# Optimization experiments

Measured on AMD Instinct MI355X. Metric: run time of the kernel, lower is better.

Reference implementation:

```python
import jax, jax.numpy as jnp
import numpy as np

HIDDEN = 1024
NUM_HEAD = 16
HEAD_DIM = HIDDEN // NUM_HEAD


def setup_inputs() -> dict:
    key = jax.random.key(0)
    ks = jax.random.split(key, 12)
    bs, seq = 4, 2048
    inp = {
        'srcQ': jax.random.normal(ks[0], (bs, seq, HIDDEN), jnp.float32),
        'srcK': jax.random.normal(ks[1], (bs, seq, HIDDEN), jnp.float32),
        'srcV': jax.random.normal(ks[2], (bs, seq, HIDDEN), jnp.float32),
        'mask': jnp.ones((bs, 1, 1, seq), jnp.int32),
        'Wq': jax.random.normal(ks[3], (HIDDEN, HIDDEN), jnp.float32) * 0.02,
        'bq': jnp.zeros((HIDDEN,), jnp.float32),
        'Wk': jax.random.normal(ks[4], (HIDDEN, HIDDEN), jnp.float32) * 0.02,
        'bk': jnp.zeros((HIDDEN,), jnp.float32),
        'Wv': jax.random.normal(ks[5], (HIDDEN, HIDDEN), jnp.float32) * 0.02,
        'bv': jnp.zeros((HIDDEN,), jnp.float32),
        'Wo': jax.random.normal(ks[6], (HIDDEN, HIDDEN), jnp.float32) * 0.02,
        'bo': jnp.zeros((HIDDEN,), jnp.float32),
    }
    return inp


def _split_heads(x):
    # [bs, seq, hidden] -> [bs, num_head, seq, head_dim]
    bs, seq, _ = x.shape
    return x.reshape(bs, seq, NUM_HEAD, HEAD_DIM).transpose(0, 2, 1, 3)


def reference(srcQ, srcK, srcV, mask, Wq, bq, Wk, bk, Wv, bv, Wo, bo):
    Q = _split_heads(srcQ @ Wq + bq)
    K = _split_heads(srcK @ Wk + bk)
    V = _split_heads(srcV @ Wv + bv)
    # NOTE: original module applies NO 1/sqrt(d) scaling (scale tensor unused)
    scores = jnp.einsum('bhqd,bhkd->bhqk', Q, K)
    scores = jnp.where(mask == 0, jnp.float32(-10000.0), scores)
    attn = jax.nn.softmax(scores, axis=-1)  # dropout is identity in eval
    out = jnp.einsum('bhqk,bhkd->bhqd', attn, V)
    bs, _, seq, _ = out.shape
    out = out.transpose(0, 2, 1, 3).reshape(bs, seq, HIDDEN)
    return out @ Wo + bo
```

## Files before the change

### kernel.cpp

```cpp
#include <hip/hip_runtime.h>

typedef short bf16x8 __attribute__((ext_vector_type(8)));
typedef short bf16x4 __attribute__((ext_vector_type(4)));
typedef float f32x4 __attribute__((ext_vector_type(4)));
typedef unsigned short ushort8 __attribute__((ext_vector_type(8)));
typedef unsigned short ushort4v __attribute__((ext_vector_type(4)));
typedef unsigned int uint4v __attribute__((ext_vector_type(4)));
typedef float float4v __attribute__((ext_vector_type(4)));

#define LOG2E 1.4426950408889634f
#define MASKED_VAL -14426.950408889634f

__device__ __forceinline__ unsigned short f2bf(float f) {
  unsigned u = __builtin_bit_cast(unsigned, f);
  u = u + 0x7fffu + ((u >> 16) & 1u);
  return (unsigned short)(u >> 16);
}

__device__ __forceinline__ unsigned pk2(float a, float b) {
  unsigned r;
  asm("v_cvt_pk_bf16_f32 %0, %1, %2" : "=v"(r) : "v"(a), "v"(b));
  return r;
}

__device__ __forceinline__ float exp2a(float x) {
  float r;
  asm("v_exp_f32 %0, %1" : "=v"(r) : "v"(x));
  return r;
}

__device__ __forceinline__ void gload16(const void* g, void* l) {
  __builtin_amdgcn_global_load_lds(
      (const __attribute__((address_space(1))) unsigned int*)g,
      (__attribute__((address_space(3))) unsigned int*)l, 16, 0, 0);
}

__global__ __launch_bounds__(256) void transpose_w4(const float* __restrict__ W0,
                                                    const float* __restrict__ W1,
                                                    const float* __restrict__ W2,
                                                    const float* __restrict__ W3,
                                                    unsigned short* __restrict__ Wt) {
  __shared__ float tile[32][33];
  const int z = blockIdx.z;
  const float* W = (z == 0) ? W0 : (z == 1) ? W1 : (z == 2) ? W2 : W3;
  unsigned short* o = Wt + (size_t)z * (1 << 20);
  int bx = blockIdx.x * 32;
  int by = blockIdx.y * 32;
  int tx = threadIdx.x & 31;
  int ty = threadIdx.x >> 5;
#pragma unroll
  for (int j = 0; j < 32; j += 8)
    tile[ty + j][tx] = W[(size_t)(by + ty + j) * 1024 + bx + tx];
  __syncthreads();
#pragma unroll
  for (int j = 0; j < 32; j += 8)
    o[(size_t)(bx + ty + j) * 1024 + by + tx] = f2bf(tile[tx][ty + j]);
}

__global__ __launch_bounds__(256, 3) void gemm_qkv(
    const float* __restrict__ srcQ, const float* __restrict__ srcK,
    const float* __restrict__ srcV, const unsigned short* __restrict__ Wt,
    const float* __restrict__ bq, const float* __restrict__ bk,
    const float* __restrict__ bv, unsigned short* __restrict__ Qb,
    unsigned short* __restrict__ Kb, unsigned short* __restrict__ Vt) {
  __shared__ __align__(16) unsigned short As[3][128 * 32];
  __shared__ __align__(16) unsigned short Bs[3][128 * 32];
  const int K = 1024, N = 1024;
  const int chunk = blockIdx.x >> 9;
  const int inner = blockIdx.x & 511;
  const int x = inner & 7, i = inner >> 3;
  const int bm = (x << 3) + (i >> 3);
  const int bn = i & 7;
  const float* Af = (chunk == 0) ? srcQ : (chunk == 1) ? srcK : srcV;
  const unsigned short* Bt = Wt + (size_t)chunk * (1 << 20);
  const float* bias = (chunk == 0) ? bq : (chunk == 1) ? bk : bv;
  const float scale = (chunk == 0) ? LOG2E : 1.0f;
  const int t = threadIdx.x;
  const int lane = t & 63, wid = t >> 6;
  const int wr = wid >> 1, wc = wid & 1;
  const int lr = lane & 15, lg = lane >> 4;
  f32x4 acc[4][4] = {};
  const size_t baseA = (size_t)(bm * 128) * K;
  const size_t baseB = (size_t)(bn * 128) * K;
  const int c0 = t, c1 = t + 256;
  const size_t a0off = baseA + (size_t)(c0 >> 2) * K + (c0 & 3) * 8;
  const size_t a1off = baseA + (size_t)(c1 >> 2) * K + (c1 & 3) * 8;
  const size_t b0off = baseB + (size_t)(c0 >> 2) * K + (c0 & 3) * 8;
  const size_t b1off = baseB + (size_t)(c1 >> 2) * K + (c1 & 3) * 8;

  unsigned short* pA0 = &As[0][0];
  unsigned short* pA1 = &As[1][0];
  unsigned short* pA2 = &As[2][0];
  unsigned short* pB0 = &Bs[0][0];
  unsigned short* pB1 = &Bs[1][0];
  unsigned short* pB2 = &Bs[2][0];
  float4v fE[4], fO[4];

  auto loadA = [&](float4v* f, int ks) {
    f[0] = *(const float4v*)&Af[a0off + ks];
    f[1] = *(const float4v*)&Af[a0off + ks + 4];
    f[2] = *(const float4v*)&Af[a1off + ks];
    f[3] = *(const float4v*)&Af[a1off + ks + 4];
  };
  auto writeA = [&](const float4v* f, unsigned short* dst) {
    uint4v w0, w1;
    w0[0] = pk2(f[0][0], f[0][1]); w0[1] = pk2(f[0][2], f[0][3]);
    w0[2] = pk2(f[1][0], f[1][1]); w0[3] = pk2(f[1][2], f[1][3]);
    w1[0] = pk2(f[2][0], f[2][1]); w1[1] = pk2(f[2][2], f[2][3]);
    w1[2] = pk2(f[3][0], f[3][1]); w1[3] = pk2(f[3][2], f[3][3]);
    *(uint4v*)&dst[c0 * 8] = w0;
    *(uint4v*)&dst[c1 * 8] = w1;
  };
  auto compute = [&]() {
    bf16x8 a[4], b[4];
#pragma unroll
    for (int m = 0; m < 4; ++m)
      a[m] = *(const bf16x8*)&pA0[(wr * 64 + 16 * m + lr) * 32 + lg * 8];
#pragma unroll
    for (int n = 0; n < 4; ++n)
      b[n] = *(const bf16x8*)&pB0[(wc * 64 + 16 * n + lr) * 32 + lg * 8];
    __builtin_amdgcn_s_setprio(1);
#pragma unroll
    for (int m = 0; m < 4; ++m)
#pragma unroll
      for (int n = 0; n < 4; ++n)
        acc[m][n] = __builtin_amdgcn_mfma_f32_16x16x32_bf16(a[m], b[n], acc[m][n], 0, 0, 0);
    __builtin_amdgcn_s_setprio(0);
  };
  auto rotate = [&]() {
    unsigned short* ta = pA0; pA0 = pA1; pA1 = pA2; pA2 = ta;
    unsigned short* tb = pB0; pB0 = pB1; pB1 = pB2; pB2 = tb;
  };

  gload16(&Bt[b0off], &pB0[c0 * 8]);
  gload16(&Bt[b1off], &pB0[c1 * 8]);
  loadA(fE, 0);
  gload16(&Bt[b0off + 32], &pB1[c0 * 8]);
  gload16(&Bt[b1off + 32], &pB1[c1 * 8]);
  loadA(fO, 32);
  writeA(fE, pA0);
  asm volatile("s_waitcnt lgkmcnt(0)" ::: "memory");
  __builtin_amdgcn_s_barrier();

  for (int it = 0; it < 16; ++it) {
    const int ks0 = 64 * it;
    if (it < 15) {
      gload16(&Bt[b0off + ks0 + 64], &pB2[c0 * 8]);
      gload16(&Bt[b1off + ks0 + 64], &pB2[c1 * 8]);
      loadA(fE, ks0 + 64);
    }
    compute();
    writeA(fO, pA1);
    asm volatile("s_waitcnt lgkmcnt(0)" ::: "memory");
    __builtin_amdgcn_sched_barrier(0);
    __builtin_amdgcn_s_barrier();
    rotate();
    if (it < 15) {
      gload16(&Bt[b0off + ks0 + 96], &pB2[c0 * 8]);
      gload16(&Bt[b1off + ks0 + 96], &pB2[c1 * 8]);
      loadA(fO, ks0 + 96);
    }
    compute();
    if (it < 15) {
      writeA(fE, pA1);
      asm volatile("s_waitcnt lgkmcnt(0)" ::: "memory");
      __builtin_amdgcn_sched_barrier(0);
      __builtin_amdgcn_s_barrier();
      rotate();
    }
  }

  const int rowb = bm * 128 + wr * 64;
  const int colb = bn * 128 + wc * 64;
  if (chunk == 2) {
    const int bidx = rowb >> 11;
    const int srow = rowb & 2047;
#pragma unroll
    for (int n = 0; n < 4; ++n) {
      int col = colb + 16 * n + lr;
      float bv_ = bias[col];
#pragma unroll
      for (int m = 0; m < 4; ++m) {
        int s0 = srow + 16 * m + 4 * lg;
        ushort4v u;
#pragma unroll
        for (int r = 0; r < 4; ++r) u[r] = f2bf(acc[m][n][r] + bv_);
        *(ushort4v*)&Vt[((size_t)(bidx * 1024 + col)) * 2048 + s0] = u;
      }
    }
  } else {
    unsigned short* C = (chunk == 0) ? Qb : Kb;
#pragma unroll
    for (int n = 0; n < 4; ++n) {
      int col = colb + 16 * n + lr;
      float bv_ = bias[col];
#pragma unroll
      for (int m = 0; m < 4; ++m) {
        int row0 = rowb + 16 * m + 4 * lg;
#pragma unroll
        for (int r = 0; r < 4; ++r)
          C[(size_t)(row0 + r) * N + col] = f2bf((acc[m][n][r] + bv_) * scale);
      }
    }
  }
}

__global__ __launch_bounds__(256, 3) void gemm_out(const unsigned short* __restrict__ A,
                                                   const unsigned short* __restrict__ Bt,
                                                   const float* __restrict__ bias,
                                                   float* __restrict__ C) {
  __shared__ __align__(16) unsigned short As[3][128 * 32];
  __shared__ __align__(16) unsigned short Bs[3][128 * 32];
  const int K = 1024, N = 1024;
  const int x = blockIdx.x & 7, i = blockIdx.x >> 3;
  const int bm = (x << 3) + (i >> 3);
  const int bn = i & 7;
  const int t = threadIdx.x;
  const int lane = t & 63, wid = t >> 6;
  const int wr = wid >> 1, wc = wid & 1;
  const int lr = lane & 15, lg = lane >> 4;
  f32x4 acc[4][4] = {};
  const size_t baseA = (size_t)(bm * 128) * K;
  const size_t baseB = (size_t)(bn * 128) * K;
  const int c0 = t, c1 = t + 256;
  const size_t a0off = baseA + (size_t)(c0 >> 2) * K + (c0 & 3) * 8;
  const size_t a1off = baseA + (size_t)(c1 >> 2) * K + (c1 & 3) * 8;
  const size_t b0off = baseB + (size_t)(c0 >> 2) * K + (c0 & 3) * 8;
  const size_t b1off = baseB + (size_t)(c1 >> 2) * K + (c1 & 3) * 8;

  unsigned short* pA0 = &As[0][0];
  unsigned short* pA1 = &As[1][0];
  unsigned short* pA2 = &As[2][0];
  unsigned short* pB0 = &Bs[0][0];
  unsigned short* pB1 = &Bs[1][0];
  unsigned short* pB2 = &Bs[2][0];

  auto issue = [&](int ks, unsigned short* dA, unsigned short* dB) {
    gload16(&A[a0off + ks], &dA[c0 * 8]);
    gload16(&A[a1off + ks], &dA[c1 * 8]);
    gload16(&Bt[b0off + ks], &dB[c0 * 8]);
    gload16(&Bt[b1off + ks], &dB[c1 * 8]);
  };
  auto rotate = [&]() {
    unsigned short* ta = pA0; pA0 = pA1; pA1 = pA2; pA2 = ta;
    unsigned short* tb = pB0; pB0 = pB1; pB1 = pB2; pB2 = tb;
  };

  issue(0, pA0, pB0);
  issue(32, pA1, pB1);
  asm volatile("s_waitcnt vmcnt(4)" ::: "memory");
  __builtin_amdgcn_sched_barrier(0);
  __builtin_amdgcn_s_barrier();

  for (int tt = 0; tt < 32; ++tt) {
    if (tt < 30) issue(32 * tt + 64, pA2, pB2);
    bf16x8 a[4], b[4];
#pragma unroll
    for (int m = 0; m < 4; ++m)
      a[m] = *(const bf16x8*)&pA0[(wr * 64 + 16 * m + lr) * 32 + lg * 8];
#pragma unroll
    for (int n = 0; n < 4; ++n)
      b[n] = *(const bf16x8*)&pB0[(wc * 64 + 16 * n + lr) * 32 + lg * 8];
    __builtin_amdgcn_s_setprio(1);
#pragma unroll
    for (int m = 0; m < 4; ++m)
#pragma unroll
      for (int n = 0; n < 4; ++n)
        acc[m][n] = __builtin_amdgcn_mfma_f32_16x16x32_bf16(a[m], b[n], acc[m][n], 0, 0, 0);
    __builtin_amdgcn_s_setprio(0);
    if (tt < 31) {
      if (tt < 30) {
        asm volatile("s_waitcnt vmcnt(4)" ::: "memory");
      } else {
        asm volatile("s_waitcnt vmcnt(0)" ::: "memory");
      }
      __builtin_amdgcn_sched_barrier(0);
      __builtin_amdgcn_s_barrier();
      rotate();
    }
  }

  const int rowb = bm * 128 + wr * 64;
  const int colb = bn * 128 + wc * 64;
#pragma unroll
  for (int n = 0; n < 4; ++n) {
    int col = colb + 16 * n + lr;
    float bv = bias[col];
#pragma unroll
    for (int m = 0; m < 4; ++m) {
      int row0 = rowb + 16 * m + 4 * lg;
#pragma unroll
      for (int r = 0; r < 4; ++r)
        C[(size_t)(row0 + r) * N + col] = acc[m][n][r] + bv;
    }
  }
}

__global__ __launch_bounds__(512, 4) void attn_kernel(
    const unsigned short* __restrict__ Q, const unsigned short* __restrict__ K,
    const unsigned short* __restrict__ V, const int* __restrict__ mask,
    unsigned short* __restrict__ ctx) {
  __shared__ __align__(16) unsigned short pool[16384];
  __shared__ int s_any[8];
  unsigned short* Kbuf0 = pool;
  unsigned short* Kbuf1 = pool + 4096;
  unsigned short* Vbuf0 = pool + 8192;
  unsigned short* Vbuf1 = pool + 12288;
  const int g = blockIdx.x;
  const int bid = (g & 7) * 64 + (g >> 3);
  const int qb = bid & 7, h = (bid >> 3) & 15, b = bid >> 7;
  const int t = threadIdx.x;
  const int lane = t & 63, wid = t >> 6;
  const int lr = lane & 15, lg = lane >> 4;
  const size_t rowQ0 = (size_t)(b * 2048 + qb * 256);
  const int hcol = h * 64;
  const size_t vrow0 = (size_t)((b * 16 + h) * 64) * 2048;

  const int row_s = t >> 3, pos_s = t & 7;
  const size_t ksrc = (size_t)(b * 2048 + row_s) * 1024 + hcol + ((pos_s ^ (row_s & 7)) << 3);
  const size_t vsrc = vrow0 + (size_t)row_s * 2048 + ((pos_s ^ ((row_s >> 1) & 7)) << 3);
  const int ldso = t * 8;

#pragma unroll
  for (int i = 0; i < 4; ++i) {
    int ci = t + 512 * i;
    int row = ci >> 3, pos = ci & 7;
    gload16(&Q[(rowQ0 + row) * 1024 + hcol + ((pos ^ (row & 7)) << 3)], &pool[ci * 8]);
  }
  const int* mb = mask + b * 2048;
  int4 mv0 = *(const int4*)&mb[t * 4];
  int bad = (mv0.x == 0) | (mv0.y == 0) | (mv0.z == 0) | (mv0.w == 0);
  unsigned long long bb = __ballot(bad);
  if (lane == 0) s_any[wid] = (bb != 0ULL);
  __syncthreads();
  bf16x8 aq[2][2];
#pragma unroll
  for (int m = 0; m < 2; ++m)
#pragma unroll
    for (int kd = 0; kd < 2; ++kd) {
      int row = wid * 32 + 16 * m + lr;
      int ch = (4 * kd + lg) ^ (lr & 7);
      aq[m][kd] = *(const bf16x8*)&pool[row * 64 + ch * 8];
    }
  int anyi = 0;
#pragma unroll
  for (int w = 0; w < 8; ++w) anyi |= s_any[w];
  const bool anymask = anyi != 0;
  __syncthreads();
  gload16(&K[ksrc], &Kbuf0[ldso]);
  gload16(&V[vsrc], &Vbuf0[ldso]);
  __syncthreads();

  f32x4 o[2][4] = {};
  f32x4 ol[2] = {};
  const short oneb = 0x3F80;
  const bf16x8 ones8 = {oneb, oneb, oneb, oneb, oneb, oneb, oneb, oneb};
  const f32x4 zero4 = {0.f, 0.f, 0.f, 0.f};
  const int ch0 = (lg ^ (lr & 7)) * 8;
  const int ch1 = ((4 + lg) ^ (lr & 7)) * 8;
  const int sw = lr >> 1;

  for (int kb = 0; kb < 32; ++kb) {
    const int bi = kb & 1;
    const unsigned short* Kb_ = bi ? Kbuf1 : Kbuf0;
    const unsigned short* Vb_ = bi ? Vbuf1 : Vbuf0;
    unsigned short* Kn_ = bi ? Kbuf0 : Kbuf1;
    unsigned short* Vn_ = bi ? Vbuf0 : Vbuf1;
    if (kb + 1 < 32) {
      gload16(&K[ksrc + (size_t)(kb + 1) * 64 * 1024], &Kn_[ldso]);
      gload16(&V[vsrc + (size_t)(kb + 1) * 64], &Vn_[ldso]);
    }
    f32x4 s[2][4];
    __builtin_amdgcn_s_setprio(1);
#pragma unroll
    for (int n = 0; n < 4; ++n) {
      bf16x8 k0 = *(const bf16x8*)&Kb_[(16 * n + lr) * 64 + ch0];
      bf16x8 k1 = *(const bf16x8*)&Kb_[(16 * n + lr) * 64 + ch1];
      f32x4 t0 = __builtin_amdgcn_mfma_f32_16x16x32_bf16(k0, aq[0][0], zero4, 0, 0, 0);
      s[0][n] = __builtin_amdgcn_mfma_f32_16x16x32_bf16(k1, aq[0][1], t0, 0, 0, 0);
      f32x4 t1 = __builtin_amdgcn_mfma_f32_16x16x32_bf16(k0, aq[1][0], zero4, 0, 0, 0);
      s[1][n] = __builtin_amdgcn_mfma_f32_16x16x32_bf16(k1, aq[1][1], t1, 0, 0, 0);
    }
    __builtin_amdgcn_s_setprio(0);
    if (anymask) {
      const int* mrow = mb + kb * 64;
#pragma unroll
      for (int n = 0; n < 4; ++n) {
        int4 mv = *(const int4*)&mrow[16 * n + 4 * lg];
        int mm[4] = {mv.x, mv.y, mv.z, mv.w};
#pragma unroll
        for (int r = 0; r < 4; ++r)
          if (mm[r] == 0) { s[0][n][r] = MASKED_VAL; s[1][n][r] = MASKED_VAL; }
      }
    }
#pragma unroll
    for (int m = 0; m < 2; ++m)
#pragma unroll
      for (int n = 0; n < 4; ++n)
#pragma unroll
        for (int r = 0; r < 4; ++r) s[m][n][r] = exp2a(s[m][n][r]);
#pragma unroll
    for (int kk = 0; kk < 2; ++kk) {
      bf16x8 pf[2];
#pragma unroll
      for (int m = 0; m < 2; ++m) {
        uint4v u;
        u[0] = pk2(s[m][2 * kk][0], s[m][2 * kk][1]);
        u[1] = pk2(s[m][2 * kk][2], s[m][2 * kk][3]);
        u[2] = pk2(s[m][2 * kk + 1][0], s[m][2 * kk + 1][1]);
        u[3] = pk2(s[m][2 * kk + 1][2], s[m][2 * kk + 1][3]);
        pf[m] = __builtin_bit_cast(bf16x8, u);
      }
      __builtin_amdgcn_s_setprio(1);
      ol[0] = __builtin_amdgcn_mfma_f32_16x16x32_bf16(ones8, pf[0], ol[0], 0, 0, 0);
      ol[1] = __builtin_amdgcn_mfma_f32_16x16x32_bf16(ones8, pf[1], ol[1], 0, 0, 0);
      const int p0 = (4 * kk + (lg >> 1)) ^ sw;
      const int base0 = lr * 64 + p0 * 8 + (lg & 1) * 4;
      const int base1 = lr * 64 + (p0 ^ 2) * 8 + (lg & 1) * 4;
#pragma unroll
      for (int dn = 0; dn < 4; ++dn) {
        bf16x4 v0 = *(const bf16x4*)&Vb_[base0 + dn * 1024];
        bf16x4 v1 = *(const bf16x4*)&Vb_[base1 + dn * 1024];
        bf16x8 vb = __builtin_shufflevector(v0, v1, 0, 1, 2, 3, 4, 5, 6, 7);
#pragma unroll
        for (int m = 0; m < 2; ++m)
          o[m][dn] = __builtin_amdgcn_mfma_f32_16x16x32_bf16(vb, pf[m], o[m][dn], 0, 0, 0);
      }
      __builtin_amdgcn_s_setprio(0);
    }
    __syncthreads();
  }
#pragma unroll
  for (int m = 0; m < 2; ++m) {
    float inv = 1.f / ol[m][0];
    size_t q = rowQ0 + wid * 32 + 16 * m + lr;
#pragma unroll
    for (int dn = 0; dn < 4; ++dn) {
      ushort4v u;
#pragma unroll
      for (int r = 0; r < 4; ++r) u[r] = f2bf(o[m][dn][r] * inv);
      *(ushort4v*)&ctx[q * 1024 + hcol + 16 * dn + 4 * lg] = u;
    }
  }
}

extern "C" void kernel_launch(void* const* d_in, const int* in_sizes, int n_in,
                              void* d_out, int out_size, void* d_ws, size_t ws_size,
                              hipStream_t stream) {
  const float* srcQ = (const float*)d_in[0];
  const float* srcK = (const float*)d_in[1];
  const float* srcV = (const float*)d_in[2];
  const int*   mask = (const int*)d_in[3];
  const float* Wq = (const float*)d_in[4];
  const float* bq = (const float*)d_in[5];
  const float* Wk = (const float*)d_in[6];
  const float* bk = (const float*)d_in[7];
  const float* Wv = (const float*)d_in[8];
  const float* bv = (const float*)d_in[9];
  const float* Wo = (const float*)d_in[10];
  const float* bo = (const float*)d_in[11];
  float* out = (float*)d_out;

  char* ws = (char*)d_ws;
  unsigned short* ctx = (unsigned short*)(ws);
  unsigned short* Qb  = (unsigned short*)(ws + (size_t)(16 << 20));
  unsigned short* Kb  = (unsigned short*)(ws + (size_t)(32 << 20));
  unsigned short* Vt  = (unsigned short*)(ws + (size_t)(48 << 20));
  unsigned short* Wt  = (unsigned short*)(ws + (size_t)(64 << 20));

  transpose_w4<<<dim3(32, 32, 4), 256, 0, stream>>>(Wq, Wk, Wv, Wo, Wt);

  gemm_qkv<<<1536, 256, 0, stream>>>(srcQ, srcK, srcV, Wt, bq, bk, bv, Qb, Kb, Vt);

  attn_kernel<<<512, 512, 0, stream>>>(Qb, Kb, Vt, mask, ctx);

  gemm_out<<<512, 256, 0, stream>>>(ctx, Wt + 3 * (1 << 20), bo, out);
}
```

Before: 177.9 us.

## Pre-pack weights in MFMA fragment order and load B directly to registers

The weight preprocessing kernel now writes the bf16 weights in a layout that matches the per-lane MFMA B-fragment order, instead of a plain transpose. Both GEMMs drop the shared-memory B buffers and load B fragments straight from global memory into registers, double-buffered across k-steps. This removes the LDS traffic and space used for B, which may raise occupancy, but each wave now fetches its own B fragments from global memory/L2. It also adds register pressure and longer global-load latency on the critical path.

```diff
diff --git a/kernel.cpp b/kernel.cpp
--- a/kernel.cpp
+++ b/kernel.cpp
@@ -35,15 +35,15 @@
       (__attribute__((address_space(3))) unsigned int*)l, 16, 0, 0);
 }
 
-__global__ __launch_bounds__(256) void transpose_w4(const float* __restrict__ W0,
-                                                    const float* __restrict__ W1,
-                                                    const float* __restrict__ W2,
-                                                    const float* __restrict__ W3,
-                                                    unsigned short* __restrict__ Wt) {
+__global__ __launch_bounds__(256) void pack_w4(const float* __restrict__ W0,
+                                               const float* __restrict__ W1,
+                                               const float* __restrict__ W2,
+                                               const float* __restrict__ W3,
+                                               unsigned short* __restrict__ P) {
   __shared__ float tile[32][33];
   const int z = blockIdx.z;
   const float* W = (z == 0) ? W0 : (z == 1) ? W1 : (z == 2) ? W2 : W3;
-  unsigned short* o = Wt + (size_t)z * (1 << 20);
+  unsigned short* o = P + (size_t)z * (1 << 20);
   int bx = blockIdx.x * 32;
   int by = blockIdx.y * 32;
   int tx = threadIdx.x & 31;
@@ -52,19 +52,28 @@
   for (int j = 0; j < 32; j += 8)
     tile[ty + j][tx] = W[(size_t)(by + ty + j) * 1024 + bx + tx];
   __syncthreads();
-#pragma unroll
-  for (int j = 0; j < 32; j += 8)
-    o[(size_t)(bx + ty + j) * 1024 + by + tx] = f2bf(tile[tx][ty + j]);
+  const int t = threadIdx.x;
+  if (t < 128) {
+    int col_l = t & 31, kg = t >> 5;
+    int col = bx + col_l;
+    ushort8 v;
+#pragma unroll
+    for (int j = 0; j < 8; ++j) v[j] = f2bf(tile[kg * 8 + j][col_l]);
+    int bn = col >> 7, cl = col & 127;
+    int wc = cl >> 6, n = (cl >> 4) & 3, lr = cl & 15;
+    int ks = by >> 5;
+    size_t off = (size_t)(bn * 32 + ks) * 4096 + (wc * 4 + n) * 512 + (kg * 16 + lr) * 8;
+    *(ushort8*)&o[off] = v;
+  }
 }
 
 __global__ __launch_bounds__(256, 3) void gemm_qkv(
     const float* __restrict__ srcQ, const float* __restrict__ srcK,
-    const float* __restrict__ srcV, const unsigned short* __restrict__ Wt,
+    const float* __restrict__ srcV, const unsigned short* __restrict__ Wp,
     const float* __restrict__ bq, const float* __restrict__ bk,
     const float* __restrict__ bv, unsigned short* __restrict__ Qb,
     unsigned short* __restrict__ Kb, unsigned short* __restrict__ Vt) {
   __shared__ __align__(16) unsigned short As[3][128 * 32];
-  __shared__ __align__(16) unsigned short Bs[3][128 * 32];
   const int K = 1024, N = 1024;
   const int chunk = blockIdx.x >> 9;
   const int inner = blockIdx.x & 511;
@@ -72,7 +81,7 @@
   const int bm = (x << 3) + (i >> 3);
   const int bn = i & 7;
   const float* Af = (chunk == 0) ? srcQ : (chunk == 1) ? srcK : srcV;
-  const unsigned short* Bt = Wt + (size_t)chunk * (1 << 20);
+  const unsigned short* Pk = Wp + (size_t)chunk * (1 << 20);
   const float* bias = (chunk == 0) ? bq : (chunk == 1) ? bk : bv;
   const float scale = (chunk == 0) ? LOG2E : 1.0f;
   const int t = threadIdx.x;
@@ -81,26 +90,30 @@
   const int lr = lane & 15, lg = lane >> 4;
   f32x4 acc[4][4] = {};
   const size_t baseA = (size_t)(bm * 128) * K;
-  const size_t baseB = (size_t)(bn * 128) * K;
   const int c0 = t, c1 = t + 256;
   const size_t a0off = baseA + (size_t)(c0 >> 2) * K + (c0 & 3) * 8;
   const size_t a1off = baseA + (size_t)(c1 >> 2) * K + (c1 & 3) * 8;
-  const size_t b0off = baseB + (size_t)(c0 >> 2) * K + (c0 & 3) * 8;
-  const size_t b1off = baseB + (size_t)(c1 >> 2) * K + (c1 & 3) * 8;
+  size_t bo[4];
+#pragma unroll
+  for (int n = 0; n < 4; ++n)
+    bo[n] = (size_t)(bn * 32) * 4096 + (size_t)(wc * 4 + n) * 512 + (size_t)lane * 8;
 
   unsigned short* pA0 = &As[0][0];
   unsigned short* pA1 = &As[1][0];
   unsigned short* pA2 = &As[2][0];
-  unsigned short* pB0 = &Bs[0][0];
-  unsigned short* pB1 = &Bs[1][0];
-  unsigned short* pB2 = &Bs[2][0];
   float4v fE[4], fO[4];
-
-  auto loadA = [&](float4v* f, int ks) {
-    f[0] = *(const float4v*)&Af[a0off + ks];
-    f[1] = *(const float4v*)&Af[a0off + ks + 4];
-    f[2] = *(const float4v*)&Af[a1off + ks];
-    f[3] = *(const float4v*)&Af[a1off + ks + 4];
+  bf16x8 bE[4], bO[4];
+
+  auto loadA = [&](float4v* f, int ke) {
+    f[0] = *(const float4v*)&Af[a0off + ke];
+    f[1] = *(const float4v*)&Af[a0off + ke + 4];
+    f[2] = *(const float4v*)&Af[a1off + ke];
+    f[3] = *(const float4v*)&Af[a1off + ke + 4];
+  };
+  auto loadB = [&](bf16x8* b, int ks) {
+#pragma unroll
+    for (int n = 0; n < 4; ++n)
+      b[n] = *(const bf16x8*)&Pk[bo[n] + (size_t)ks * 4096];
   };
   auto writeA = [&](const float4v* f, unsigned short* dst) {
     uint4v w0, w1;
@@ -111,14 +124,11 @@
     *(uint4v*)&dst[c0 * 8] = w0;
     *(uint4v*)&dst[c1 * 8] = w1;
   };
-  auto compute = [&]() {
-    bf16x8 a[4], b[4];
+  auto compute = [&](const bf16x8* b) {
+    bf16x8 a[4];
 #pragma unroll
     for (int m = 0; m < 4; ++m)
       a[m] = *(const bf16x8*)&pA0[(wr * 64 + 16 * m + lr) * 32 + lg * 8];
-#pragma unroll
-    for (int n = 0; n < 4; ++n)
-      b[n] = *(const bf16x8*)&pB0[(wc * 64 + 16 * n + lr) * 32 + lg * 8];
     __builtin_amdgcn_s_setprio(1);
 #pragma unroll
     for (int m = 0; m < 4; ++m)
@@ -129,38 +139,29 @@
   };
   auto rotate = [&]() {
     unsigned short* ta = pA0; pA0 = pA1; pA1 = pA2; pA2 = ta;
-    unsigned short* tb = pB0; pB0 = pB1; pB1 = pB2; pB2 = tb;
-  };
-
-  gload16(&Bt[b0off], &pB0[c0 * 8]);
-  gload16(&Bt[b1off], &pB0[c1 * 8]);
+  };
+
   loadA(fE, 0);
-  gload16(&Bt[b0off + 32], &pB1[c0 * 8]);
-  gload16(&Bt[b1off + 32], &pB1[c1 * 8]);
+  loadB(bE, 0);
   loadA(fO, 32);
+  loadB(bO, 1);
   writeA(fE, pA0);
   asm volatile("s_waitcnt lgkmcnt(0)" ::: "memory");
   __builtin_amdgcn_s_barrier();
 
   for (int it = 0; it < 16; ++it) {
-    const int ks0 = 64 * it;
-    if (it < 15) {
-      gload16(&Bt[b0off + ks0 + 64], &pB2[c0 * 8]);
-      gload16(&Bt[b1off + ks0 + 64], &pB2[c1 * 8]);
-      loadA(fE, ks0 + 64);
-    }
-    compute();
+    const int t0 = 2 * it;
+    if (it < 15) loadA(fE, 32 * (t0 + 2));
+    compute(bE);
+    if (t0 + 2 < 32) loadB(bE, t0 + 2);
     writeA(fO, pA1);
     asm volatile("s_waitcnt lgkmcnt(0)" ::: "memory");
     __builtin_amdgcn_sched_barrier(0);
     __builtin_amdgcn_s_barrier();
     rotate();
-    if (it < 15) {
-      gload16(&Bt[b0off + ks0 + 96], &pB2[c0 * 8]);
-      gload16(&Bt[b1off + ks0 + 96], &pB2[c1 * 8]);
-      loadA(fO, ks0 + 96);
-    }
-    compute();
+    if (it < 15) loadA(fO, 32 * (t0 + 3));
+    compute(bO);
+    if (t0 + 3 < 32) loadB(bO, t0 + 3);
     if (it < 15) {
       writeA(fE, pA1);
       asm volatile("s_waitcnt lgkmcnt(0)" ::: "memory");
@@ -206,11 +207,10 @@
 }
 
 __global__ __launch_bounds__(256, 3) void gemm_out(const unsigned short* __restrict__ A,
-                                                   const unsigned short* __restrict__ Bt,
+                                                   const unsigned short* __restrict__ Bp,
                                                    const float* __restrict__ bias,
                                                    float* __restrict__ C) {
   __shared__ __align__(16) unsigned short As[3][128 * 32];
-  __shared__ __align__(16) unsigned short Bs[3][128 * 32];
   const int K = 1024, N = 1024;
   const int x = blockIdx.x & 7, i = blockIdx.x >> 3;
   const int bm = (x << 3) + (i >> 3);
@@ -221,46 +221,33 @@
   const int lr = lane & 15, lg = lane >> 4;
   f32x4 acc[4][4] = {};
   const size_t baseA = (size_t)(bm * 128) * K;
-  const size_t baseB = (size_t)(bn * 128) * K;
   const int c0 = t, c1 = t + 256;
   const size_t a0off = baseA + (size_t)(c0 >> 2) * K + (c0 & 3) * 8;
   const size_t a1off = baseA + (size_t)(c1 >> 2) * K + (c1 & 3) * 8;
-  const size_t b0off = baseB + (size_t)(c0 >> 2) * K + (c0 & 3) * 8;
-  const size_t b1off = baseB + (size_t)(c1 >> 2) * K + (c1 & 3) * 8;
+  size_t bo[4];
+#pragma unroll
+  for (int n = 0; n < 4; ++n)
+    bo[n] = (size_t)(bn * 32) * 4096 + (size_t)(wc * 4 + n) * 512 + (size_t)lane * 8;
 
   unsigned short* pA0 = &As[0][0];
   unsigned short* pA1 = &As[1][0];
   unsigned short* pA2 = &As[2][0];
-  unsigned short* pB0 = &Bs[0][0];
-  unsigned short* pB1 = &Bs[1][0];
-  unsigned short* pB2 = &Bs[2][0];
-
-  auto issue = [&](int ks, unsigned short* dA, unsigned short* dB) {
-    gload16(&A[a0off + ks], &dA[c0 * 8]);
-    gload16(&A[a1off + ks], &dA[c1 * 8]);
-    gload16(&Bt[b0off + ks], &dB[c0 * 8]);
-    gload16(&Bt[b1off + ks], &dB[c1 * 8]);
-  };
-  auto rotate = [&]() {
-    unsigned short* ta = pA0; pA0 = pA1; pA1 = pA2; pA2 = ta;
-    unsigned short* tb = pB0; pB0 = pB1; pB1 = pB2; pB2 = tb;
-  };
-
-  issue(0, pA0, pB0);
-  issue(32, pA1, pB1);
-  asm volatile("s_waitcnt vmcnt(4)" ::: "memory");
-  __builtin_amdgcn_sched_barrier(0);
-  __builtin_amdgcn_s_barrier();
-
-  for (int tt = 0; tt < 32; ++tt) {
-    if (tt < 30) issue(32 * tt + 64, pA2, pB2);
-    bf16x8 a[4], b[4];
+  bf16x8 bE[4], bO[4];
+
+  auto dmaA = [&](int ks, unsigned short* dA) {
+    gload16(&A[a0off + 32 * ks], &dA[c0 * 8]);
+    gload16(&A[a1off + 32 * ks], &dA[c1 * 8]);
+  };
+  auto loadB = [&](bf16x8* b, int ks) {
+#pragma unroll
+    for (int n = 0; n < 4; ++n)
+      b[n] = *(const bf16x8*)&Bp[bo[n] + (size_t)ks * 4096];
+  };
+  auto compute = [&](const bf16x8* b) {
+    bf16x8 a[4];
 #pragma unroll
     for (int m = 0; m < 4; ++m)
       a[m] = *(const bf16x8*)&pA0[(wr * 64 + 16 * m + lr) * 32 + lg * 8];
-#pragma unroll
-    for (int n = 0; n < 4; ++n)
-      b[n] = *(const bf16x8*)&pB0[(wc * 64 + 16 * n + lr) * 32 + lg * 8];
     __builtin_amdgcn_s_setprio(1);
 #pragma unroll
     for (int m = 0; m < 4; ++m)
@@ -268,9 +255,40 @@
       for (int n = 0; n < 4; ++n)
         acc[m][n] = __builtin_amdgcn_mfma_f32_16x16x32_bf16(a[m], b[n], acc[m][n], 0, 0, 0);
     __builtin_amdgcn_s_setprio(0);
-    if (tt < 31) {
-      if (tt < 30) {
-        asm volatile("s_waitcnt vmcnt(4)" ::: "memory");
+  };
+  auto rotate = [&]() {
+    unsigned short* ta = pA0; pA0 = pA1; pA1 = pA2; pA2 = ta;
+  };
+
+  dmaA(0, pA0);
+  dmaA(1, pA1);
+  loadB(bE, 0);
+  loadB(bO, 1);
+  asm volatile("s_waitcnt vmcnt(10)" ::: "memory");
+  __builtin_amdgcn_sched_barrier(0);
+  __builtin_amdgcn_s_barrier();
+
+  for (int it = 0; it < 16; ++it) {
+    const int t0 = 2 * it;
+    if (t0 + 2 < 32) dmaA(t0 + 2, pA2);
+    compute(bE);
+    if (t0 + 2 < 32) loadB(bE, t0 + 2);
+    {
+      if (t0 < 30) {
+        asm volatile("s_waitcnt vmcnt(6)" ::: "memory");
+      } else {
+        asm volatile("s_waitcnt vmcnt(0)" ::: "memory");
+      }
+      __builtin_amdgcn_sched_barrier(0);
+      __builtin_amdgcn_s_barrier();
+      rotate();
+    }
+    if (t0 + 3 < 32) dmaA(t0 + 3, pA2);
+    compute(bO);
+    if (t0 + 3 < 32) loadB(bO, t0 + 3);
+    if (it < 15) {
+      if (t0 + 1 < 30) {
+        asm volatile("s_waitcnt vmcnt(6)" ::: "memory");
       } else {
         asm volatile("s_waitcnt vmcnt(0)" ::: "memory");
       }
@@ -466,13 +484,13 @@
   unsigned short* Qb  = (unsigned short*)(ws + (size_t)(16 << 20));
   unsigned short* Kb  = (unsigned short*)(ws + (size_t)(32 << 20));
   unsigned short* Vt  = (unsigned short*)(ws + (size_t)(48 << 20));
-  unsigned short* Wt  = (unsigned short*)(ws + (size_t)(64 << 20));
-
-  transpose_w4<<<dim3(32, 32, 4), 256, 0, stream>>>(Wq, Wk, Wv, Wo, Wt);
-
-  gemm_qkv<<<1536, 256, 0, stream>>>(srcQ, srcK, srcV, Wt, bq, bk, bv, Qb, Kb, Vt);
+  unsigned short* Wp  = (unsigned short*)(ws + (size_t)(64 << 20));
+
+  pack_w4<<<dim3(32, 32, 4), 256, 0, stream>>>(Wq, Wk, Wv, Wo, Wp);
+
+  gemm_qkv<<<1536, 256, 0, stream>>>(srcQ, srcK, srcV, Wp, bq, bk, bv, Qb, Kb, Vt);
 
   attn_kernel<<<512, 512, 0, stream>>>(Qb, Kb, Vt, mask, ctx);
 
-  gemm_out<<<512, 256, 0, stream>>>(ctx, Wt + 3 * (1 << 20), bo, out);
-}
+  gemm_out<<<512, 256, 0, stream>>>(ctx, Wp + 3 * (1 << 20), bo, out);
+}
```

After: 170.5 us, median of 2. 1.04x faster.
